# Kernel tuning notes

Measured on AMD Instinct MI355X. Metric: run time of the kernel, lower is better.

## Reference

```python
import jax, jax.numpy as jnp
import numpy as np

N = 50000      # nodes
E = 600000     # edges
IN = 128       # input_dim
HID = 128      # hidden_dim
OUT = 128      # output_dim
H = 4          # heads
D = OUT // H   # head dim
R = 4          # rel_num
L = 2          # n_layer
M = 10000      # len(idx)
EPS = 1e-5


def setup_inputs() -> dict:
    key = jax.random.key(0)
    ks = jax.random.split(key, 16)
    f = jax.random.normal
    inp = {
        "x": f(ks[0], (N, IN), jnp.float32),
        "proj_w": f(ks[1], (IN, HID), jnp.float32) / np.sqrt(IN).astype(np.float32),
        "proj_b": jnp.zeros((HID,), jnp.float32),
        "bn_gamma": jnp.ones((HID,), jnp.float32),
        "bn_beta": jnp.zeros((HID,), jnp.float32),
        # per-layer HGTConv params (stacked on leading L axis; layer0 in=HID, layer1 in=OUT, equal here)
        "q_w": f(ks[2], (L, HID, OUT), jnp.float32) / np.sqrt(HID).astype(np.float32),
        "q_b": jnp.zeros((L, OUT), jnp.float32),
        "k_w": f(ks[3], (L, HID, OUT), jnp.float32) / np.sqrt(HID).astype(np.float32),
        "k_b": jnp.zeros((L, OUT), jnp.float32),
        "v_w": f(ks[4], (L, HID, OUT), jnp.float32) / np.sqrt(HID).astype(np.float32),
        "v_b": jnp.zeros((L, OUT), jnp.float32),
        "a_w": f(ks[5], (L, OUT, OUT), jnp.float32) / np.sqrt(OUT).astype(np.float32),
        "a_b": jnp.zeros((L, OUT), jnp.float32),
        "skip": jnp.ones((L,), jnp.float32),
        "a_rel": f(ks[6], (L, R, H, D, D), jnp.float32) / np.sqrt(D).astype(np.float32),
        "m_rel": f(ks[7], (L, R, H, D, D), jnp.float32) / np.sqrt(D).astype(np.float32),
        "p_rel": jnp.ones((L, R, H), jnp.float32),
        "edge_index": jax.random.randint(ks[8], (2, E), 0, N, dtype=jnp.int32),
        "edge_type": jax.random.randint(ks[9], (E,), 0, R, dtype=jnp.int32),
        "idx": jax.random.randint(ks[10], (M,), 0, N, dtype=jnp.int32),
    }
    return inp


def _hgt_forward(x, proj_w, proj_b, bn_gamma, bn_beta, q_w, q_b, k_w, k_b, v_w, v_b,
                 a_w, a_b, skip, a_rel, m_rel, p_rel, edge_index, edge_type, idx):
    # proj + BatchNorm1d (training-mode batch statistics, biased variance)
    h = x @ proj_w + proj_b
    mu = h.mean(axis=0)
    var = jnp.mean((h - mu) ** 2, axis=0)
    h = (h - mu) * jax.lax.rsqrt(var + EPS) * bn_gamma + bn_beta

    src, dst = edge_index[0], edge_index[1]          # message from src(j) to dst(i)
    seg = dst * R + edge_type                        # per-(dst, relation) softmax segments
    scale = np.float32(1.0 / np.sqrt(D))

    for l in range(L):
        q = (h @ q_w[l] + q_b[l]).reshape(N, H, D)
        k = (h @ k_w[l] + k_b[l]).reshape(N, H, D)
        v = (h @ v_w[l] + v_b[l]).reshape(N, H, D)
        # relation-specific key/value transforms for every node/relation: [N,R,H,D]
        k_all = jnp.einsum('nhd,rhde->nrhe', k, a_rel[l])
        v_all = jnp.einsum('nhd,rhde->nrhe', v, m_rel[l])
        k_e = k_all[src, edge_type]                  # [E,H,D]
        v_e = v_all[src, edge_type]                  # [E,H,D]
        score = jnp.sum(q[dst] * k_e, axis=-1) * p_rel[l][edge_type] * scale  # [E,H]
        # per-relation segment softmax over incoming edges of each dst node
        smax = jax.ops.segment_max(score, seg, num_segments=N * R)
        e = jnp.exp(score - smax[seg])
        denom = jax.ops.segment_sum(e, seg, num_segments=N * R)
        alpha = e / denom[seg]                        # [E,H]
        out = jax.ops.segment_sum(alpha[..., None] * v_e, dst, num_segments=N)
        out = out.reshape(N, OUT)
        out = jax.nn.gelu(out, approximate=False) @ a_w[l] + a_b[l]
        b = jax.nn.sigmoid(skip[l])                   # learned skip gate
        h = b * out + (1.0 - b) * h                   # dims match -> residual mix
    return h[idx]


def reference(x, proj_w, proj_b, bn_gamma, bn_beta, q_w, q_b, k_w, k_b, v_w, v_b,
              a_w, a_b, skip, a_rel, m_rel, p_rel, edge_index, edge_type, idx):
    return _hgt_forward(x, proj_w, proj_b, bn_gamma, bn_beta, q_w, q_b, k_w, k_b,
                        v_w, v_b, a_w, a_b, skip, a_rel, m_rel, p_rel,
                        edge_index, edge_type, idx)
```

## Files before the change

### kernel.cpp

```cpp
#include <hip/hip_runtime.h>
#include <math.h>

#define NN 50000
#define EE 600000
#define MOUT 10000
#define DEGCAP 384
#define NT4 (NN * 4)

typedef short bf16x8 __attribute__((ext_vector_type(8)));
typedef float f32x4 __attribute__((ext_vector_type(4)));

__device__ __forceinline__ unsigned short f2bf(float x) {
    unsigned int u = __float_as_uint(x);
    u = (u + 0x7FFFu + ((u >> 16) & 1u)) >> 16;
    return (unsigned short)u;
}
__device__ __forceinline__ float bf2f(unsigned int b) {
    return __uint_as_float(b << 16);
}
__device__ __forceinline__ uint4 pack8bf(float4 a, float4 b) {
    uint4 r;
    r.x = (unsigned int)f2bf(a.x) | ((unsigned int)f2bf(a.y) << 16);
    r.y = (unsigned int)f2bf(a.z) | ((unsigned int)f2bf(a.w) << 16);
    r.z = (unsigned int)f2bf(b.x) | ((unsigned int)f2bf(b.y) << 16);
    r.w = (unsigned int)f2bf(b.z) | ((unsigned int)f2bf(b.w) << 16);
    return r;
}

__global__ __launch_bounds__(256) void prep_kernel(
    const float* __restrict__ proj_w, const float* __restrict__ a_w,
    const float* __restrict__ q_w, const float* __restrict__ q_b,
    const float* __restrict__ a_rel,
    const float* __restrict__ k_w, const float* __restrict__ k_b,
    const float* __restrict__ v_w, const float* __restrict__ v_b,
    const float* __restrict__ m_rel, const float* __restrict__ p_rel,
    unsigned short* __restrict__ wt_pa, unsigned short* __restrict__ qkvw,
    float* __restrict__ fbias, unsigned short* __restrict__ msg_wt,
    int* __restrict__ cnt, float* __restrict__ stats)
{
    const int b = blockIdx.x, t = threadIdx.x;
    if (b < 192) {
        int wi = b >> 6;
        int flat = (b & 63) * 256 + t;
        int n = flat >> 7, c = flat & 127;
        const float* src = (wi == 0) ? proj_w : (wi == 1) ? a_w : a_w + 16384;
        wt_pa[(size_t)wi * 16384 + n * 128 + c] = f2bf(src[c * 128 + n]);
    } else if (b < 960) {
        int q = b - 192;
        int l = q >= 384 ? 1 : 0;
        int flat = (q - l * 384) * 256 + t;
        int nrow = flat >> 7, c = flat & 127;
        unsigned short* wt = qkvw + (size_t)l * 98304;
        float* fb = fbias + l * 768;
        if (nrow < 512) {
            int r = nrow >> 7, hh = (nrow >> 5) & 3, d = nrow & 31;
            float prl = p_rel[l * 16 + r * 4 + hh] * 0.17677669529663687f;
            const float* qwc = q_w + (size_t)l * 16384 + c * 128 + hh * 32;
            const float* ar  = a_rel + (size_t)(l * 4 + r) * 4096 + hh * 1024 + d * 32;
            float s = 0.f;
            #pragma unroll 8
            for (int e = 0; e < 32; ++e) s += qwc[e] * ar[e];
            wt[(size_t)nrow * 128 + c] = f2bf(s * prl);
            if (c == 0) {
                const float* qb = q_b + l * 128 + hh * 32;
                float bb = 0.f;
                #pragma unroll 8
                for (int e = 0; e < 32; ++e) bb += qb[e] * ar[e];
                fb[nrow] = bb * prl;
            }
        } else {
            int j = nrow - 512;
            int tt = j >> 2, s = j & 3;
            int col = 2 * tt + (s & 1);
            const float* w  = (s < 2) ? k_w : v_w;
            const float* bb = (s < 2) ? k_b : v_b;
            wt[(size_t)nrow * 128 + c] = f2bf(w[(size_t)l * 16384 + c * 128 + col]);
            if (c == 0) fb[nrow] = bb[l * 128 + col];
        }
    } else if (b < 1472) {
        int q = b - 960;
        int l = q >= 256 ? 1 : 0;
        int flat = (q - l * 256) * 256 + t;
        int n = flat >> 9, kk = flat & 511;
        int h = n >> 5, e = n & 31;
        int r = kk >> 7, h2 = (kk >> 5) & 3, d = kk & 31;
        float val = (h2 == h) ? m_rel[(size_t)(l * 4 + r) * 4096 + h * 1024 + d * 32 + e] : 0.f;
        msg_wt[(size_t)l * 65536 + (size_t)n * 512 + kk] = f2bf(val);
    } else {
        int i = (b - 1472) * 256 + t;
        if (i < NT4) cnt[i] = 0;
        if (i < 256) stats[i] = 0.f;
    }
}

__global__ __launch_bounds__(256) void hist_kernel(const int* __restrict__ ei,
    const int* __restrict__ et, int* __restrict__ cnt, int E)
{
    int e = blockIdx.x * 256 + threadIdx.x;
    if (e < E) atomicAdd(&cnt[ei[E + e] * 4 + et[e]], 1);
}

__global__ __launch_bounds__(256) void scan_block_kernel(const int* __restrict__ cnt,
    int* __restrict__ excl, int* __restrict__ bsum, int n)
{
    __shared__ int tmp[256];
    int i = blockIdx.x * 256 + threadIdx.x;
    int v = (i < n) ? cnt[i] : 0;
    tmp[threadIdx.x] = v;
    __syncthreads();
    for (int ofs = 1; ofs < 256; ofs <<= 1) {
        int t = (threadIdx.x >= ofs) ? tmp[threadIdx.x - ofs] : 0;
        __syncthreads();
        tmp[threadIdx.x] += t;
        __syncthreads();
    }
    if (i < n) excl[i] = tmp[threadIdx.x] - v;
    if (threadIdx.x == 255) bsum[blockIdx.x] = tmp[255];
}

__global__ __launch_bounds__(256) void scan_add_kernel(int* __restrict__ excl,
    const int* __restrict__ bsum, int* __restrict__ fill,
    int* __restrict__ maskz, int n, int total)
{
    __shared__ int red[256];
    const int b = blockIdx.x;
    int partial = 0;
    for (int j = threadIdx.x; j < b; j += 256) partial += bsum[j];
    red[threadIdx.x] = partial;
    __syncthreads();
    for (int ofs = 128; ofs > 0; ofs >>= 1) {
        if (threadIdx.x < ofs) red[threadIdx.x] += red[threadIdx.x + ofs];
        __syncthreads();
    }
    int prefix = red[0];
    int i = b * 256 + threadIdx.x;
    if (i < n) {
        int o = excl[i] + prefix;
        excl[i] = o;
        fill[i] = o;
    }
    if (i < 12500) maskz[i] = 0;
    if (b == 0 && threadIdx.x == 0) excl[n] = total;
}

__global__ __launch_bounds__(256) void scatter_kernel(const int* __restrict__ ei,
    const int* __restrict__ et, int* __restrict__ fill, int* __restrict__ pack,
    const int* __restrict__ idxp, unsigned char* __restrict__ mask, int Mo, int E)
{
    int e = blockIdx.x * 256 + threadIdx.x;
    if (e >= E) return;
    int seg = ei[E + e] * 4 + et[e];
    int p = atomicAdd(&fill[seg], 1);
    pack[p] = ei[e];
    if (e < Mo) mask[idxp[e]] = 1;
}

__global__ __launch_bounds__(256) void projstats_kernel(
    const float* __restrict__ X, const unsigned short* __restrict__ Wt,
    const float* __restrict__ bias, unsigned short* __restrict__ Cb,
    float* __restrict__ stats, int M)
{
    __shared__ unsigned short As[128 * 40];
    __shared__ unsigned short Bs[128 * 40];
    const int t = threadIdx.x;
    const int wave = t >> 6, lane = t & 63;
    const int quad = lane >> 4, l16 = lane & 15;
    const int row0 = blockIdx.x * 128;
    const int wr = (wave & 1) * 64, wc = (wave >> 1) * 64;
    const int sr = t >> 1, sc = (t & 1) * 16;
    const int grow = row0 + sr;

    f32x4 acc[4][4];
    #pragma unroll
    for (int i = 0; i < 4; ++i)
        #pragma unroll
        for (int j = 0; j < 4; ++j)
            acc[i][j] = (f32x4){0.f, 0.f, 0.f, 0.f};

    uint4 av0 = make_uint4(0,0,0,0), av1 = av0, bv0, bv1;
    if (grow < M) {
        const float4* ap = (const float4*)(X + (size_t)grow * 128 + sc);
        av0 = pack8bf(ap[0], ap[1]);
        av1 = pack8bf(ap[2], ap[3]);
    }
    {
        const uint4* bp = (const uint4*)(Wt + (size_t)sr * 128 + sc);
        bv0 = bp[0]; bv1 = bp[1];
    }
    for (int it = 0; it < 4; ++it) {
        __syncthreads();
        *(uint4*)(As + sr * 40 + sc)     = av0;
        *(uint4*)(As + sr * 40 + sc + 8) = av1;
        *(uint4*)(Bs + sr * 40 + sc)     = bv0;
        *(uint4*)(Bs + sr * 40 + sc + 8) = bv1;
        __syncthreads();
        if (it + 1 < 4) {
            int kb = (it + 1) * 32;
            if (grow < M) {
                const float4* ap = (const float4*)(X + (size_t)grow * 128 + kb + sc);
                av0 = pack8bf(ap[0], ap[1]);
                av1 = pack8bf(ap[2], ap[3]);
            }
            const uint4* bp = (const uint4*)(Wt + (size_t)sr * 128 + kb + sc);
            bv0 = bp[0]; bv1 = bp[1];
        }
        bf16x8 af[4], bfr[4];
        #pragma unroll
        for (int f = 0; f < 4; ++f) {
            af[f]  = *(const bf16x8*)(As + (wr + f * 16 + l16) * 40 + quad * 8);
            bfr[f] = *(const bf16x8*)(Bs + (wc + f * 16 + l16) * 40 + quad * 8);
        }
        #pragma unroll
        for (int fr = 0; fr < 4; ++fr)
            #pragma unroll
            for (int fc = 0; fc < 4; ++fc)
                acc[fr][fc] = __builtin_amdgcn_mfma_f32_16x16x32_bf16(
                    af[fr], bfr[fc], acc[fr][fc], 0, 0, 0);
    }

    #pragma unroll
    for (int fc = 0; fc < 4; ++fc) {
        const int col = wc + fc * 16 + l16;
        const float bv = bias[col];
        float s = 0.f, s2 = 0.f;
        #pragma unroll
        for (int fr = 0; fr < 4; ++fr)
            #pragma unroll
            for (int reg = 0; reg < 4; ++reg) {
                int row = row0 + wr + fr * 16 + quad * 4 + reg;
                float val = acc[fr][fc][reg] + bv;
                if (row < M) {
                    Cb[(size_t)row * 128 + col] = f2bf(val);
                    s += val; s2 += val * val;
                }
            }
        s  += __shfl_xor(s, 16);  s  += __shfl_xor(s, 32);
        s2 += __shfl_xor(s2, 16); s2 += __shfl_xor(s2, 32);
        if (quad == 0) {
            atomicAdd(&stats[col], s);
            atomicAdd(&stats[128 + col], s2);
        }
    }
}

__global__ __launch_bounds__(256) void bnqkv_kernel(
    const unsigned short* __restrict__ hb, const float* __restrict__ stats,
    const float* __restrict__ gamma, const float* __restrict__ beta,
    const unsigned short* __restrict__ qkvw, const float* __restrict__ fbias,
    unsigned short* __restrict__ hn, unsigned short* __restrict__ qkv, int M)
{
    __shared__ unsigned short hS[128 * 136];
    __shared__ unsigned short Bs[128 * 40];
    __shared__ float mulS[128], addS[128];
    const int t = threadIdx.x;
    const int row0 = blockIdx.x * 128;
    if (t < 128) {
        float invN = 1.f / 50000.f;
        float mu = stats[t] * invN;
        float var = stats[128 + t] * invN - mu * mu;
        float ml = rsqrtf(var + 1e-5f) * gamma[t];
        mulS[t] = ml;
        addS[t] = beta[t] - mu * ml;
    }
    __syncthreads();
    #pragma unroll
    for (int u = 0; u < 8; ++u) {
        int li = t + u * 256;
        int row = li >> 4, c0 = (li & 15) * 8;
        uint4 pk = make_uint4(0, 0, 0, 0);
        if (row0 + row < M)
            pk = ((const uint4*)(hb + (size_t)(row0 + row) * 128))[li & 15];
        unsigned int w[4] = {pk.x, pk.y, pk.z, pk.w};
        uint4 o;
        unsigned int ov[4];
        #pragma unroll
        for (int g = 0; g < 4; ++g) {
            int c = c0 + g * 2;
            float a0 = bf2f(w[g] & 0xFFFFu) * mulS[c]     + addS[c];
            float a1 = bf2f(w[g] >> 16)     * mulS[c + 1] + addS[c + 1];
            ov[g] = (unsigned int)f2bf(a0) | ((unsigned int)f2bf(a1) << 16);
        }
        o.x = ov[0]; o.y = ov[1]; o.z = ov[2]; o.w = ov[3];
        *(uint4*)(hS + row * 136 + c0) = o;
        if (row0 + row < M)
            ((uint4*)(hn + (size_t)(row0 + row) * 128))[li & 15] = o;
    }
    __syncthreads();

    const int wave = t >> 6, lane = t & 63;
    const int quad = lane >> 4, l16 = lane & 15;
    const int wr = (wave & 1) * 64, wcl = (wave >> 1) * 64;
    const int sr = t >> 1, scc = (t & 1) * 16;

    uint4 pv0, pv1;
    {
        const uint4* bp = (const uint4*)(qkvw + (size_t)sr * 128 + scc);
        pv0 = bp[0]; pv1 = bp[1];
    }
    for (int ch = 0; ch < 6; ++ch) {
        f32x4 acc[4][4];
        #pragma unroll
        for (int i = 0; i < 4; ++i)
            #pragma unroll
            for (int j = 0; j < 4; ++j)
                acc[i][j] = (f32x4){0.f, 0.f, 0.f, 0.f};
        for (int it = 0; it < 4; ++it) {
            __syncthreads();
            *(uint4*)(Bs + sr * 40 + scc)     = pv0;
            *(uint4*)(Bs + sr * 40 + scc + 8) = pv1;
            __syncthreads();
            int nit = it + 1, nch = ch;
            if (nit == 4) { nit = 0; ++nch; }
            if (nch < 6) {
                const uint4* bp = (const uint4*)(qkvw + (size_t)(nch * 128 + sr) * 128 + nit * 32 + scc);
                pv0 = bp[0]; pv1 = bp[1];
            }
            bf16x8 af[4], bfr[4];
            #pragma unroll
            for (int f = 0; f < 4; ++f) {
                af[f]  = *(const bf16x8*)(hS + (wr + f * 16 + l16) * 136 + it * 32 + quad * 8);
                bfr[f] = *(const bf16x8*)(Bs + (wcl + f * 16 + l16) * 40 + quad * 8);
            }
            #pragma unroll
            for (int fr = 0; fr < 4; ++fr)
                #pragma unroll
                for (int fc = 0; fc < 4; ++fc)
                    acc[fr][fc] = __builtin_amdgcn_mfma_f32_16x16x32_bf16(
                        af[fr], bfr[fc], acc[fr][fc], 0, 0, 0);
        }
        float b4[4];
        #pragma unroll
        for (int fc = 0; fc < 4; ++fc)
            b4[fc] = fbias[ch * 128 + wcl + fc * 16 + l16];
        #pragma unroll
        for (int fr = 0; fr < 4; ++fr)
            #pragma unroll
            for (int reg = 0; reg < 4; ++reg) {
                int row = row0 + wr + fr * 16 + quad * 4 + reg;
                if (row >= M) continue;
                #pragma unroll
                for (int fc = 0; fc < 4; ++fc) {
                    int col = ch * 128 + wcl + fc * 16 + l16;
                    qkv[(size_t)row * 768 + col] = f2bf(acc[fr][fc][reg] + b4[fc]);
                }
            }
    }
}

__global__ __launch_bounds__(256) void agg_fused_kernel(
    const unsigned short* __restrict__ qkv,
    const unsigned short* __restrict__ qbuf, int qpitch,
    const int* __restrict__ off4, const int* __restrict__ pack,
    const int* __restrict__ rowmap, unsigned short* __restrict__ aggb, int count)
{
    __shared__ int spack[4][DEGCAP];
    const int wv = threadIdx.x >> 6;
    const int lane = threadIdx.x & 63;
    const int unit = blockIdx.x * 4 + wv;
    if (unit >= count) return;
    const int node = rowmap ? __builtin_amdgcn_readfirstlane(rowmap[unit]) : unit;

    const unsigned int* qrow = (const unsigned int*)(qbuf + (size_t)unit * qpitch);
    unsigned int quv[4];
    #pragma unroll
    for (int r = 0; r < 4; ++r) quv[r] = qrow[r * 64 + lane];

    int off_r[5];
    #pragma unroll
    for (int i = 0; i < 5; ++i)
        off_r[i] = __builtin_amdgcn_readfirstlane(off4[node * 4 + i]);
    const int beg = off_r[0];
    const int deg = off_r[4] - beg;
    const bool cached = deg <= DEGCAP;

    if (cached) {
        for (int i = lane; i < deg; i += 64) spack[wv][i] = pack[beg + i];
        asm volatile("s_waitcnt vmcnt(0) lgkmcnt(0)" ::: "memory");
    }

    unsigned int outw[4];
    #pragma unroll
    for (int r = 0; r < 4; ++r) {
        float qx = bf2f(quv[r] & 0xFFFFu);
        float qy = bf2f(quv[r] >> 16);
        float den = 0.f, ax = 0.f, ay = 0.f;

        if (cached) {
            const int rb = off_r[r] - beg, re = off_r[r + 1] - beg;
            for (int i = rb; i < re; i += 4) {
                unsigned int ku[4], vu[4];
                #pragma unroll
                for (int j = 0; j < 4; ++j) {
                    int ii = i + j; if (ii >= re) ii = re - 1;
                    int src = spack[wv][ii];
                    uint2 kv = *(const uint2*)(qkv + (size_t)src * 768 + 512 + lane * 4);
                    ku[j] = kv.x; vu[j] = kv.y;
                }
                float p[4];
                #pragma unroll
                for (int j = 0; j < 4; ++j)
                    p[j] = qx * bf2f(ku[j] & 0xFFFFu) + qy * bf2f(ku[j] >> 16);
                #pragma unroll
                for (int j = 0; j < 4; ++j) {
                    p[j] += __shfl_xor(p[j], 1); p[j] += __shfl_xor(p[j], 2);
                    p[j] += __shfl_xor(p[j], 4); p[j] += __shfl_xor(p[j], 8);
                }
                #pragma unroll
                for (int j = 0; j < 4; ++j) {
                    float s = fminf(fmaxf(p[j], -80.f), 80.f);
                    float e = __expf(s);
                    if (i + j >= re) e = 0.f;
                    den += e;
                    ax += e * bf2f(vu[j] & 0xFFFFu);
                    ay += e * bf2f(vu[j] >> 16);
                }
            }
        } else {
            for (int pp = off_r[r]; pp < off_r[r + 1]; ++pp) {
                int src = __builtin_amdgcn_readfirstlane(pack[pp]);
                uint2 kv = *(const uint2*)(qkv + (size_t)src * 768 + 512 + lane * 4);
                float p0 = qx * bf2f(kv.x & 0xFFFFu) + qy * bf2f(kv.x >> 16);
                p0 += __shfl_xor(p0, 1); p0 += __shfl_xor(p0, 2);
                p0 += __shfl_xor(p0, 4); p0 += __shfl_xor(p0, 8);
                float e = __expf(fminf(fmaxf(p0, -80.f), 80.f));
                den += e;
                ax += e * bf2f(kv.y & 0xFFFFu);
                ay += e * bf2f(kv.y >> 16);
            }
        }
        float inv = den > 0.f ? 1.f / den : 0.f;
        outw[r] = (unsigned int)f2bf(ax * inv) | ((unsigned int)f2bf(ay * inv) << 16);
    }
    unsigned int* op = (unsigned int*)(aggb + (size_t)unit * 512);
    #pragma unroll
    for (int r = 0; r < 4; ++r) op[r * 64 + lane] = outw[r];
}

__global__ __launch_bounds__(256) void mlpqkv_kernel(
    const unsigned short* __restrict__ A, const unsigned short* __restrict__ W3t,
    const unsigned short* __restrict__ AWt, const float* __restrict__ a_bias,
    const float* __restrict__ skipv, const unsigned short* __restrict__ hres,
    const unsigned short* __restrict__ qkvw1, const float* __restrict__ fbias1,
    const unsigned char* __restrict__ mask,
    unsigned short* __restrict__ h1, unsigned short* __restrict__ qkv, int M)
{
    __shared__ unsigned short As[128 * 40];
    __shared__ unsigned short Bs[128 * 40];
    __shared__ unsigned short msgS[128 * 136];
    const int t = threadIdx.x;
    const int wave = t >> 6, lane = t & 63;
    const int quad = lane >> 4, l16 = lane & 15;
    const int row0 = blockIdx.x * 128;
    const int wr = (wave & 1) * 64, wcl = (wave >> 1) * 64;
    const int sr = t >> 1, scc = (t & 1) * 16;
    const int grow = row0 + sr;
    const bool rvalid = grow < M;

    f32x4 acc[4][4];
    #pragma unroll
    for (int i = 0; i < 4; ++i)
        #pragma unroll
        for (int j = 0; j < 4; ++j)
            acc[i][j] = (f32x4){0.f, 0.f, 0.f, 0.f};

    uint4 av0 = make_uint4(0,0,0,0), av1 = av0, bv0, bv1;
    if (rvalid) {
        const uint4* ap = (const uint4*)(A + (size_t)grow * 512 + scc);
        av0 = ap[0]; av1 = ap[1];
    }
    {
        const uint4* bp = (const uint4*)(W3t + (size_t)sr * 512 + scc);
        bv0 = bp[0]; bv1 = bp[1];
    }
    for (int it = 0; it < 16; ++it) {
        __syncthreads();
        *(uint4*)(As + sr * 40 + scc)     = av0;
        *(uint4*)(As + sr * 40 + scc + 8) = av1;
        *(uint4*)(Bs + sr * 40 + scc)     = bv0;
        *(uint4*)(Bs + sr * 40 + scc + 8) = bv1;
        __syncthreads();
        if (it + 1 < 16) {
            int kb = (it + 1) * 32;
            if (rvalid) {
                const uint4* ap = (const uint4*)(A + (size_t)grow * 512 + kb + scc);
                av0 = ap[0]; av1 = ap[1];
            }
            const uint4* bp = (const uint4*)(W3t + (size_t)sr * 512 + kb + scc);
            bv0 = bp[0]; bv1 = bp[1];
        }
        bf16x8 af[4], bfr[4];
        #pragma unroll
        for (int f = 0; f < 4; ++f) {
            af[f]  = *(const bf16x8*)(As + (wr + f * 16 + l16) * 40 + quad * 8);
            bfr[f] = *(const bf16x8*)(Bs + (wcl + f * 16 + l16) * 40 + quad * 8);
        }
        #pragma unroll
        for (int fr = 0; fr < 4; ++fr)
            #pragma unroll
            for (int fc = 0; fc < 4; ++fc)
                acc[fr][fc] = __builtin_amdgcn_mfma_f32_16x16x32_bf16(
                    af[fr], bfr[fc], acc[fr][fc], 0, 0, 0);
    }

    #pragma unroll
    for (int fr = 0; fr < 4; ++fr)
        #pragma unroll
        for (int reg = 0; reg < 4; ++reg) {
            int rl = wr + fr * 16 + quad * 4 + reg;
            #pragma unroll
            for (int fc = 0; fc < 4; ++fc) {
                int col = wcl + fc * 16 + l16;
                float v = acc[fr][fc][reg];
                float gl = 0.5f * v * (1.f + erff(v * 0.70710678118654752f));
                msgS[rl * 136 + col] = f2bf(gl);
            }
        }

    f32x4 acc2[4][4];
    #pragma unroll
    for (int i = 0; i < 4; ++i)
        #pragma unroll
        for (int j = 0; j < 4; ++j)
            acc2[i][j] = (f32x4){0.f, 0.f, 0.f, 0.f};
    uint4 pv0, pv1;
    {
        const uint4* bp = (const uint4*)(AWt + (size_t)sr * 128 + scc);
        pv0 = bp[0]; pv1 = bp[1];
    }
    for (int it = 0; it < 4; ++it) {
        __syncthreads();
        *(uint4*)(Bs + sr * 40 + scc)     = pv0;
        *(uint4*)(Bs + sr * 40 + scc + 8) = pv1;
        __syncthreads();
        if (it + 1 < 4) {
            const uint4* bp = (const uint4*)(AWt + (size_t)sr * 128 + (it + 1) * 32 + scc);
            pv0 = bp[0]; pv1 = bp[1];
        } else {
            const uint4* bp = (const uint4*)(qkvw1 + (size_t)(4 * 128 + sr) * 128 + scc);
            pv0 = bp[0]; pv1 = bp[1];
        }
        bf16x8 af[4], bfr[4];
        #pragma unroll
        for (int f = 0; f < 4; ++f) {
            af[f]  = *(const bf16x8*)(msgS + (wr + f * 16 + l16) * 136 + it * 32 + quad * 8);
            bfr[f] = *(const bf16x8*)(Bs + (wcl + f * 16 + l16) * 40 + quad * 8);
        }
        #pragma unroll
        for (int fr = 0; fr < 4; ++fr)
            #pragma unroll
            for (int fc = 0; fc < 4; ++fc)
                acc2[fr][fc] = __builtin_amdgcn_mfma_f32_16x16x32_bf16(
                    af[fr], bfr[fc], acc2[fr][fc], 0, 0, 0);
    }

    const float gate = 1.f / (1.f + __expf(-skipv[0]));
    __syncthreads();
    #pragma unroll
    for (int fr = 0; fr < 4; ++fr)
        #pragma unroll
        for (int reg = 0; reg < 4; ++reg) {
            int rl = wr + fr * 16 + quad * 4 + reg;
            int row = row0 + rl;
            const bool rv = row < M;
            const bool mw = rv && mask[row];
            #pragma unroll
            for (int fc = 0; fc < 4; ++fc) {
                int col = wcl + fc * 16 + l16;
                float val = acc2[fr][fc][reg] + a_bias[col];
                float nv = val;
                if (rv) {
                    unsigned int hu = hres[(size_t)row * 128 + col];
                    nv = gate * val + (1.f - gate) * bf2f(hu);
                    if (mw) h1[(size_t)row * 128 + col] = f2bf(nv);
                }
                msgS[rl * 136 + col] = f2bf(nv);
            }
        }

    for (int ch = 4; ch < 6; ++ch) {
        f32x4 acc3[4][4];
        #pragma unroll
        for (int i = 0; i < 4; ++i)
            #pragma unroll
            for (int j = 0; j < 4; ++j)
                acc3[i][j] = (f32x4){0.f, 0.f, 0.f, 0.f};
        for (int it = 0; it < 4; ++it) {
            __syncthreads();
            *(uint4*)(Bs + sr * 40 + scc)     = pv0;
            *(uint4*)(Bs + sr * 40 + scc + 8) = pv1;
            __syncthreads();
            int nit = it + 1, nch = ch;
            if (nit == 4) { nit = 0; ++nch; }
            if (nch < 6) {
                const uint4* bp = (const uint4*)(qkvw1 + (size_t)(nch * 128 + sr) * 128 + nit * 32 + scc);
                pv0 = bp[0]; pv1 = bp[1];
            }
            bf16x8 af[4], bfr[4];
            #pragma unroll
            for (int f = 0; f < 4; ++f) {
                af[f]  = *(const bf16x8*)(msgS + (wr + f * 16 + l16) * 136 + it * 32 + quad * 8);
                bfr[f] = *(const bf16x8*)(Bs + (wcl + f * 16 + l16) * 40 + quad * 8);
            }
            #pragma unroll
            for (int fr = 0; fr < 4; ++fr)
                #pragma unroll
                for (int fc = 0; fc < 4; ++fc)
                    acc3[fr][fc] = __builtin_amdgcn_mfma_f32_16x16x32_bf16(
                        af[fr], bfr[fc], acc3[fr][fc], 0, 0, 0);
        }
        float b4[4];
        #pragma unroll
        for (int fc = 0; fc < 4; ++fc)
            b4[fc] = fbias1[ch * 128 + wcl + fc * 16 + l16];
        #pragma unroll
        for (int fr = 0; fr < 4; ++fr)
            #pragma unroll
            for (int reg = 0; reg < 4; ++reg) {
                int row = row0 + wr + fr * 16 + quad * 4 + reg;
                if (row >= M) continue;
                #pragma unroll
                for (int fc = 0; fc < 4; ++fc) {
                    int col = ch * 128 + wcl + fc * 16 + l16;
                    qkv[(size_t)row * 768 + col] = f2bf(acc3[fr][fc][reg] + b4[fc]);
                }
            }
    }
}

__global__ __launch_bounds__(256) void q1_kernel(
    const unsigned short* __restrict__ h1, const int* __restrict__ idxp,
    const unsigned short* __restrict__ qkvw1, const float* __restrict__ fbias1,
    unsigned short* __restrict__ q1, int M)
{
    __shared__ unsigned short hS[128 * 136];
    __shared__ unsigned short Bs[128 * 40];
    const int t = threadIdx.x;
    const int row0 = blockIdx.x * 128;
    #pragma unroll
    for (int u = 0; u < 8; ++u) {
        int li = t + u * 256;
        int row = li >> 4, c = li & 15;
        uint4 pk = make_uint4(0, 0, 0, 0);
        if (row0 + row < M) {
            int node = idxp[row0 + row];
            pk = ((const uint4*)(h1 + (size_t)node * 128))[c];
        }
        *(uint4*)(hS + row * 136 + c * 8) = pk;
    }
    __syncthreads();

    const int wave = t >> 6, lane = t & 63;
    const int quad = lane >> 4, l16 = lane & 15;
    const int wr = (wave & 1) * 64, wcl = (wave >> 1) * 64;
    const int sr = t >> 1, scc = (t & 1) * 16;
    uint4 pv0, pv1;
    {
        const uint4* bp = (const uint4*)(qkvw1 + (size_t)sr * 128 + scc);
        pv0 = bp[0]; pv1 = bp[1];
    }
    for (int ch = 0; ch < 4; ++ch) {
        f32x4 acc[4][4];
        #pragma unroll
        for (int i = 0; i < 4; ++i)
            #pragma unroll
            for (int j = 0; j < 4; ++j)
                acc[i][j] = (f32x4){0.f, 0.f, 0.f, 0.f};
        for (int it = 0; it < 4; ++it) {
            __syncthreads();
            *(uint4*)(Bs + sr * 40 + scc)     = pv0;
            *(uint4*)(Bs + sr * 40 + scc + 8) = pv1;
            __syncthreads();
            int nit = it + 1, nch = ch;
            if (nit == 4) { nit = 0; ++nch; }
            if (nch < 4) {
                const uint4* bp = (const uint4*)(qkvw1 + (size_t)(nch * 128 + sr) * 128 + nit * 32 + scc);
                pv0 = bp[0]; pv1 = bp[1];
            }
            bf16x8 af[4], bfr[4];
            #pragma unroll
            for (int f = 0; f < 4; ++f) {
                af[f]  = *(const bf16x8*)(hS + (wr + f * 16 + l16) * 136 + it * 32 + quad * 8);
                bfr[f] = *(const bf16x8*)(Bs + (wcl + f * 16 + l16) * 40 + quad * 8);
            }
            #pragma unroll
            for (int fr = 0; fr < 4; ++fr)
                #pragma unroll
                for (int fc = 0; fc < 4; ++fc)
                    acc[fr][fc] = __builtin_amdgcn_mfma_f32_16x16x32_bf16(
                        af[fr], bfr[fc], acc[fr][fc], 0, 0, 0);
        }
        float b4[4];
        #pragma unroll
        for (int fc = 0; fc < 4; ++fc)
            b4[fc] = fbias1[ch * 128 + wcl + fc * 16 + l16];
        #pragma unroll
        for (int fr = 0; fr < 4; ++fr)
            #pragma unroll
            for (int reg = 0; reg < 4; ++reg) {
                int row = row0 + wr + fr * 16 + quad * 4 + reg;
                if (row >= M) continue;
                #pragma unroll
                for (int fc = 0; fc < 4; ++fc) {
                    int col = ch * 128 + wcl + fc * 16 + l16;
                    q1[(size_t)row * 512 + col] = f2bf(acc[fr][fc][reg] + b4[fc]);
                }
            }
    }
}

__global__ __launch_bounds__(256) void mlp1_kernel(
    const unsigned short* __restrict__ A, const unsigned short* __restrict__ W3t,
    const unsigned short* __restrict__ AWt, const float* __restrict__ a_bias,
    const float* __restrict__ skipv, const unsigned short* __restrict__ hres,
    const int* __restrict__ rowmap, float* __restrict__ out, int M)
{
    __shared__ unsigned short As[128 * 40];
    __shared__ unsigned short Bs[128 * 40];
    __shared__ unsigned short msgS[128 * 136];
    const int t = threadIdx.x;
    const int wave = t >> 6, lane = t & 63;
    const int quad = lane >> 4, l16 = lane & 15;
    const int row0 = blockIdx.x * 128;
    const int wr = (wave & 1) * 64, wcl = (wave >> 1) * 64;
    const int sr = t >> 1, scc = (t & 1) * 16;
    const int grow = row0 + sr;
    const bool rvalid = grow < M;

    f32x4 acc[4][4];
    #pragma unroll
    for (int i = 0; i < 4; ++i)
        #pragma unroll
        for (int j = 0; j < 4; ++j)
            acc[i][j] = (f32x4){0.f, 0.f, 0.f, 0.f};

    uint4 av0 = make_uint4(0,0,0,0), av1 = av0, bv0, bv1;
    if (rvalid) {
        const uint4* ap = (const uint4*)(A + (size_t)grow * 512 + scc);
        av0 = ap[0]; av1 = ap[1];
    }
    {
        const uint4* bp = (const uint4*)(W3t + (size_t)sr * 512 + scc);
        bv0 = bp[0]; bv1 = bp[1];
    }
    for (int it = 0; it < 16; ++it) {
        __syncthreads();
        *(uint4*)(As + sr * 40 + scc)     = av0;
        *(uint4*)(As + sr * 40 + scc + 8) = av1;
        *(uint4*)(Bs + sr * 40 + scc)     = bv0;
        *(uint4*)(Bs + sr * 40 + scc + 8) = bv1;
        __syncthreads();
        if (it + 1 < 16) {
            int kb = (it + 1) * 32;
            if (rvalid) {
                const uint4* ap = (const uint4*)(A + (size_t)grow * 512 + kb + scc);
                av0 = ap[0]; av1 = ap[1];
            }
            const uint4* bp = (const uint4*)(W3t + (size_t)sr * 512 + kb + scc);
            bv0 = bp[0]; bv1 = bp[1];
        }
        bf16x8 af[4], bfr[4];
        #pragma unroll
        for (int f = 0; f < 4; ++f) {
            af[f]  = *(const bf16x8*)(As + (wr + f * 16 + l16) * 40 + quad * 8);
            bfr[f] = *(const bf16x8*)(Bs + (wcl + f * 16 + l16) * 40 + quad * 8);
        }
        #pragma unroll
        for (int fr = 0; fr < 4; ++fr)
            #pragma unroll
            for (int fc = 0; fc < 4; ++fc)
                acc[fr][fc] = __builtin_amdgcn_mfma_f32_16x16x32_bf16(
                    af[fr], bfr[fc], acc[fr][fc], 0, 0, 0);
    }

    #pragma unroll
    for (int fr = 0; fr < 4; ++fr)
        #pragma unroll
        for (int reg = 0; reg < 4; ++reg) {
            int rl = wr + fr * 16 + quad * 4 + reg;
            #pragma unroll
            for (int fc = 0; fc < 4; ++fc) {
                int col = wcl + fc * 16 + l16;
                float v = acc[fr][fc][reg];
                float gl = 0.5f * v * (1.f + erff(v * 0.70710678118654752f));
                msgS[rl * 136 + col] = f2bf(gl);
            }
        }

    f32x4 acc2[4][4];
    #pragma unroll
    for (int i = 0; i < 4; ++i)
        #pragma unroll
        for (int j = 0; j < 4; ++j)
            acc2[i][j] = (f32x4){0.f, 0.f, 0.f, 0.f};
    uint4 pv0, pv1;
    {
        const uint4* bp = (const uint4*)(AWt + (size_t)sr * 128 + scc);
        pv0 = bp[0]; pv1 = bp[1];
    }
    for (int it = 0; it < 4; ++it) {
        __syncthreads();
        *(uint4*)(Bs + sr * 40 + scc)     = pv0;
        *(uint4*)(Bs + sr * 40 + scc + 8) = pv1;
        __syncthreads();
        if (it + 1 < 4) {
            const uint4* bp = (const uint4*)(AWt + (size_t)sr * 128 + (it + 1) * 32 + scc);
            pv0 = bp[0]; pv1 = bp[1];
        }
        bf16x8 af[4], bfr[4];
        #pragma unroll
        for (int f = 0; f < 4; ++f) {
            af[f]  = *(const bf16x8*)(msgS + (wr + f * 16 + l16) * 136 + it * 32 + quad * 8);
            bfr[f] = *(const bf16x8*)(Bs + (wcl + f * 16 + l16) * 40 + quad * 8);
        }
        #pragma unroll
        for (int fr = 0; fr < 4; ++fr)
            #pragma unroll
            for (int fc = 0; fc < 4; ++fc)
                acc2[fr][fc] = __builtin_amdgcn_mfma_f32_16x16x32_bf16(
                    af[fr], bfr[fc], acc2[fr][fc], 0, 0, 0);
    }

    const float gate = 1.f / (1.f + __expf(-skipv[0]));
    #pragma unroll
    for (int fr = 0; fr < 4; ++fr)
        #pragma unroll
        for (int reg = 0; reg < 4; ++reg) {
            int row = row0 + wr + fr * 16 + quad * 4 + reg;
            if (row >= M) continue;
            int hrow = rowmap[row];
            #pragma unroll
            for (int fc = 0; fc < 4; ++fc) {
                int col = wcl + fc * 16 + l16;
                float val = acc2[fr][fc][reg] + a_bias[col];
                float nv = gate * val + (1.f - gate) * bf2f((unsigned int)hres[(size_t)hrow * 128 + col]);
                out[(size_t)row * 128 + col] = nv;
            }
        }
}

extern "C" void kernel_launch(void* const* d_in, const int* in_sizes, int n_in,
                              void* d_out, int out_size, void* d_ws, size_t ws_size,
                              hipStream_t stream)
{
    const float* x      = (const float*)d_in[0];
    const float* proj_w = (const float*)d_in[1];
    const float* proj_b = (const float*)d_in[2];
    const float* bn_g   = (const float*)d_in[3];
    const float* bn_b   = (const float*)d_in[4];
    const float* q_w    = (const float*)d_in[5];
    const float* q_b    = (const float*)d_in[6];
    const float* k_w    = (const float*)d_in[7];
    const float* k_b    = (const float*)d_in[8];
    const float* v_w    = (const float*)d_in[9];
    const float* v_b    = (const float*)d_in[10];
    const float* a_w    = (const float*)d_in[11];
    const float* a_b    = (const float*)d_in[12];
    const float* skip   = (const float*)d_in[13];
    const float* a_rel  = (const float*)d_in[14];
    const float* m_rel  = (const float*)d_in[15];
    const float* p_rel  = (const float*)d_in[16];
    const int* edge_index = (const int*)d_in[17];
    const int* edge_type  = (const int*)d_in[18];
    const int* idx        = (const int*)d_in[19];
    float* out = (float*)d_out;

    const int N = NN, E = EE;
    float* ws = (float*)d_ws;
    size_t o = 0;
    float* stats  = ws + o;  o += 256;
    float* fbias  = ws + o;  o += 2 * 768;
    int* cnt  = (int*)(ws + o); o += NT4;
    int* off4 = (int*)(ws + o); o += NT4 + 1;
    int* fill = (int*)(ws + o); o += NT4;
    int* bsum = (int*)(ws + o); o += 1024;
    int* pack = (int*)(ws + o); o += E;
    unsigned short* x_bf   = (unsigned short*)(ws + o); o += (size_t)N * 64;
    unsigned short* h_bf   = (unsigned short*)(ws + o); o += (size_t)N * 64;
    unsigned short* hn_bf  = (unsigned short*)(ws + o); o += (size_t)N * 64;
    unsigned short* h1_bf  = (unsigned short*)(ws + o); o += (size_t)N * 64;
    unsigned short* qkv_bf = (unsigned short*)(ws + o); o += (size_t)N * 384;
    unsigned short* agg_bf = (unsigned short*)(ws + o); o += (size_t)N * 256;
    unsigned short* wt_pa  = (unsigned short*)(ws + o); o += 3 * 16384 / 2;
    unsigned short* qkvw   = (unsigned short*)(ws + o); o += 2 * 98304 / 2;
    unsigned short* msg_wt = (unsigned short*)(ws + o); o += 2 * 65536 / 2;

    unsigned char* mask = (unsigned char*)cnt;
    unsigned short* q1 = x_bf;

    const int NB4 = (NT4 + 255) / 256;
    const int g = (N + 127) / 128;

    prep_kernel<<<1472 + NB4, 256, 0, stream>>>(
        proj_w, a_w, q_w, q_b, a_rel, k_w, k_b, v_w, v_b, m_rel, p_rel,
        wt_pa, qkvw, fbias, msg_wt, cnt, stats);

    hist_kernel<<<(E + 255) / 256, 256, 0, stream>>>(edge_index, edge_type, cnt, E);
    scan_block_kernel<<<NB4, 256, 0, stream>>>(cnt, off4, bsum, NT4);
    scan_add_kernel<<<NB4, 256, 0, stream>>>(off4, bsum, fill, cnt, NT4, E);
    scatter_kernel<<<(E + 255) / 256, 256, 0, stream>>>(edge_index, edge_type, fill,
                                                        pack, idx, mask, MOUT, E);

    projstats_kernel<<<g, 256, 0, stream>>>(x, wt_pa, proj_b, h_bf, stats, N);

    bnqkv_kernel<<<g, 256, 0, stream>>>(h_bf, stats, bn_g, bn_b, qkvw, fbias,
                                        hn_bf, qkv_bf, N);

    agg_fused_kernel<<<(N + 3) / 4, 256, 0, stream>>>(qkv_bf, qkv_bf, 768,
                                                      off4, pack, nullptr, agg_bf, N);

    mlpqkv_kernel<<<g, 256, 0, stream>>>(agg_bf, msg_wt, wt_pa + 16384, a_b, skip,
                                         hn_bf, qkvw + 98304, fbias + 768,
                                         mask, h1_bf, qkv_bf, N);

    q1_kernel<<<(MOUT + 127) / 128, 256, 0, stream>>>(h1_bf, idx, qkvw + 98304,
                                                      fbias + 768, q1, MOUT);

    agg_fused_kernel<<<(MOUT + 3) / 4, 256, 0, stream>>>(qkv_bf, q1, 512,
                                                         off4, pack, idx, agg_bf, MOUT);

    mlp1_kernel<<<(MOUT + 127) / 128, 256, 0, stream>>>(agg_bf, msg_wt + 65536,
                                                        wt_pa + 2 * 16384, a_b + 128,
                                                        skip + 1, h1_bf, idx, out, MOUT);
}
```

Before: 439.5 us.

## Interleave K/V in groups of four and process two edges per wave in aggregation

Changes the interleaved K/V weight column layout from pairs to groups of four, so each lane loads a 16-byte uint4 holding four K and four V values. The aggregation kernel splits the wave into two 32-lane halves that handle different edges at once, which halves the dot-product shuffle depth and doubles per-lane load width. Partial softmax sums are merged across halves with a lane-32 shuffle. The aim is fewer, wider gathers and fewer loop iterations per edge, at the cost of idle lanes on odd edge counts and an extra cross-half reduction.

```diff
diff --git a/kernel.cpp b/kernel.cpp
--- a/kernel.cpp
+++ b/kernel.cpp
@@ -70,10 +70,10 @@
             }
         } else {
             int j = nrow - 512;
-            int tt = j >> 2, s = j & 3;
-            int col = 2 * tt + (s & 1);
-            const float* w  = (s < 2) ? k_w : v_w;
-            const float* bb = (s < 2) ? k_b : v_b;
+            int tt = j >> 3, s = j & 7;
+            int col = 4 * tt + (s & 3);
+            const float* w  = (s < 4) ? k_w : v_w;
+            const float* bb = (s < 4) ? k_b : v_b;
             wt[(size_t)nrow * 128 + c] = f2bf(w[(size_t)l * 16384 + c * 128 + col]);
             if (c == 0) fb[nrow] = bb[l * 128 + col];
         }
@@ -356,14 +356,16 @@
     __shared__ int spack[4][DEGCAP];
     const int wv = threadIdx.x >> 6;
     const int lane = threadIdx.x & 63;
+    const int l32 = lane & 31;
+    const int hi = lane >> 5;
     const int unit = blockIdx.x * 4 + wv;
     if (unit >= count) return;
     const int node = rowmap ? __builtin_amdgcn_readfirstlane(rowmap[unit]) : unit;
 
-    const unsigned int* qrow = (const unsigned int*)(qbuf + (size_t)unit * qpitch);
-    unsigned int quv[4];
-    #pragma unroll
-    for (int r = 0; r < 4; ++r) quv[r] = qrow[r * 64 + lane];
+    const uint2* qrow = (const uint2*)(qbuf + (size_t)unit * qpitch);
+    uint2 quv[4];
+    #pragma unroll
+    for (int r = 0; r < 4; ++r) quv[r] = qrow[r * 32 + l32];
 
     int off_r[5];
     #pragma unroll
@@ -378,62 +380,72 @@
         asm volatile("s_waitcnt vmcnt(0) lgkmcnt(0)" ::: "memory");
     }
 
-    unsigned int outw[4];
+    uint2 outw[4];
     #pragma unroll
     for (int r = 0; r < 4; ++r) {
-        float qx = bf2f(quv[r] & 0xFFFFu);
-        float qy = bf2f(quv[r] >> 16);
-        float den = 0.f, ax = 0.f, ay = 0.f;
+        float q0 = bf2f(quv[r].x & 0xFFFFu), q1 = bf2f(quv[r].x >> 16);
+        float q2 = bf2f(quv[r].y & 0xFFFFu), q3 = bf2f(quv[r].y >> 16);
+        float den = 0.f, a0 = 0.f, a1 = 0.f, a2 = 0.f, a3 = 0.f;
 
         if (cached) {
             const int rb = off_r[r] - beg, re = off_r[r + 1] - beg;
             for (int i = rb; i < re; i += 4) {
-                unsigned int ku[4], vu[4];
-                #pragma unroll
-                for (int j = 0; j < 4; ++j) {
-                    int ii = i + j; if (ii >= re) ii = re - 1;
-                    int src = spack[wv][ii];
-                    uint2 kv = *(const uint2*)(qkv + (size_t)src * 768 + 512 + lane * 4);
-                    ku[j] = kv.x; vu[j] = kv.y;
+                int i0 = i + hi;      if (i0 >= re) i0 = re - 1;
+                int i1 = i + 2 + hi;  if (i1 >= re) i1 = re - 1;
+                int s0 = spack[wv][i0], s1 = spack[wv][i1];
+                uint4 kv0 = *(const uint4*)(qkv + (size_t)s0 * 768 + 512 + l32 * 8);
+                uint4 kv1 = *(const uint4*)(qkv + (size_t)s1 * 768 + 512 + l32 * 8);
+                {
+                    float p = q0 * bf2f(kv0.x & 0xFFFFu) + q1 * bf2f(kv0.x >> 16)
+                            + q2 * bf2f(kv0.y & 0xFFFFu) + q3 * bf2f(kv0.y >> 16);
+                    p += __shfl_xor(p, 1); p += __shfl_xor(p, 2); p += __shfl_xor(p, 4);
+                    float e = __expf(fminf(fmaxf(p, -80.f), 80.f));
+                    if (i + hi >= re) e = 0.f;
+                    den += e;
+                    a0 += e * bf2f(kv0.z & 0xFFFFu); a1 += e * bf2f(kv0.z >> 16);
+                    a2 += e * bf2f(kv0.w & 0xFFFFu); a3 += e * bf2f(kv0.w >> 16);
                 }
-                float p[4];
-                #pragma unroll
-                for (int j = 0; j < 4; ++j)
-                    p[j] = qx * bf2f(ku[j] & 0xFFFFu) + qy * bf2f(ku[j] >> 16);
-                #pragma unroll
-                for (int j = 0; j < 4; ++j) {
-                    p[j] += __shfl_xor(p[j], 1); p[j] += __shfl_xor(p[j], 2);
-                    p[j] += __shfl_xor(p[j], 4); p[j] += __shfl_xor(p[j], 8);
+                {
+                    float p = q0 * bf2f(kv1.x & 0xFFFFu) + q1 * bf2f(kv1.x >> 16)
+                            + q2 * bf2f(kv1.y & 0xFFFFu) + q3 * bf2f(kv1.y >> 16);
+                    p += __shfl_xor(p, 1); p += __shfl_xor(p, 2); p += __shfl_xor(p, 4);
+                    float e = __expf(fminf(fmaxf(p, -80.f), 80.f));
+                    if (i + 2 + hi >= re) e = 0.f;
+                    den += e;
+                    a0 += e * bf2f(kv1.z & 0xFFFFu); a1 += e * bf2f(kv1.z >> 16);
+                    a2 += e * bf2f(kv1.w & 0xFFFFu); a3 += e * bf2f(kv1.w >> 16);
                 }
-                #pragma unroll
-                for (int j = 0; j < 4; ++j) {
-                    float s = fminf(fmaxf(p[j], -80.f), 80.f);
-                    float e = __expf(s);
-                    if (i + j >= re) e = 0.f;
-                    den += e;
-                    ax += e * bf2f(vu[j] & 0xFFFFu);
-                    ay += e * bf2f(vu[j] >> 16);
-                }
             }
         } else {
-            for (int pp = off_r[r]; pp < off_r[r + 1]; ++pp) {
-                int src = __builtin_amdgcn_readfirstlane(pack[pp]);
-                uint2 kv = *(const uint2*)(qkv + (size_t)src * 768 + 512 + lane * 4);
-                float p0 = qx * bf2f(kv.x & 0xFFFFu) + qy * bf2f(kv.x >> 16);
-                p0 += __shfl_xor(p0, 1); p0 += __shfl_xor(p0, 2);
-                p0 += __shfl_xor(p0, 4); p0 += __shfl_xor(p0, 8);
-                float e = __expf(fminf(fmaxf(p0, -80.f), 80.f));
+            const int pe_end = off_r[r + 1];
+            for (int pp = off_r[r]; pp < pe_end; pp += 2) {
+                int pe = pp + hi; if (pe >= pe_end) pe = pe_end - 1;
+                int src = pack[pe];
+                uint4 kv = *(const uint4*)(qkv + (size_t)src * 768 + 512 + l32 * 8);
+                float p = q0 * bf2f(kv.x & 0xFFFFu) + q1 * bf2f(kv.x >> 16)
+                        + q2 * bf2f(kv.y & 0xFFFFu) + q3 * bf2f(kv.y >> 16);
+                p += __shfl_xor(p, 1); p += __shfl_xor(p, 2); p += __shfl_xor(p, 4);
+                float e = __expf(fminf(fmaxf(p, -80.f), 80.f));
+                if (pp + hi >= pe_end) e = 0.f;
                 den += e;
-                ax += e * bf2f(kv.y & 0xFFFFu);
-                ay += e * bf2f(kv.y >> 16);
-            }
-        }
+                a0 += e * bf2f(kv.z & 0xFFFFu); a1 += e * bf2f(kv.z >> 16);
+                a2 += e * bf2f(kv.w & 0xFFFFu); a3 += e * bf2f(kv.w >> 16);
+            }
+        }
+        den += __shfl_xor(den, 32);
+        a0  += __shfl_xor(a0, 32);
+        a1  += __shfl_xor(a1, 32);
+        a2  += __shfl_xor(a2, 32);
+        a3  += __shfl_xor(a3, 32);
         float inv = den > 0.f ? 1.f / den : 0.f;
-        outw[r] = (unsigned int)f2bf(ax * inv) | ((unsigned int)f2bf(ay * inv) << 16);
-    }
-    unsigned int* op = (unsigned int*)(aggb + (size_t)unit * 512);
-    #pragma unroll
-    for (int r = 0; r < 4; ++r) op[r * 64 + lane] = outw[r];
+        outw[r].x = (unsigned int)f2bf(a0 * inv) | ((unsigned int)f2bf(a1 * inv) << 16);
+        outw[r].y = (unsigned int)f2bf(a2 * inv) | ((unsigned int)f2bf(a3 * inv) << 16);
+    }
+    if (hi == 0) {
+        uint2* op = (uint2*)(aggb + (size_t)unit * 512);
+        #pragma unroll
+        for (int r = 0; r < 4; ++r) op[r * 32 + l32] = outw[r];
+    }
 }
 
 __global__ __launch_bounds__(256) void mlpqkv_kernel(
```

Result: no change. 442.5 us (+0.7%).
